# Performance work log

Hardware: AMD Instinct MI355X
Metric: run time of the kernel (lower is better)

## Reference

```python
import jax, jax.numpy as jnp
import numpy as np

EMBED_DIM = 1024
NUM_HEADS = 16
HEAD_DIM = EMBED_DIM // NUM_HEADS  # 64
SCALING = 0.125
T, B = 2048, 2


def setup_inputs() -> dict:
    key = jax.random.key(0)
    k_q, k_len, k_w1, k_b1, k_w2, k_b2 = jax.random.split(key, 6)
    query = jax.random.normal(k_q, (T, B, EMBED_DIM), dtype=jnp.float32)
    # realistic padding: each sequence has a valid length in [T//2, T)
    lengths = jax.random.randint(k_len, (B,), T // 2, T)
    key_padding_mask = jnp.arange(T)[None, :] >= lengths[:, None]  # [B, T] bool, True = pad
    s1 = 1.0 / np.sqrt(EMBED_DIM)
    W_in = jax.random.uniform(k_w1, (3 * EMBED_DIM, EMBED_DIM), jnp.float32, -s1, s1)
    b_in = jax.random.uniform(k_b1, (3 * EMBED_DIM,), jnp.float32, -s1, s1)
    W_out = jax.random.uniform(k_w2, (EMBED_DIM, EMBED_DIM), jnp.float32, -s1, s1)
    b_out = jax.random.uniform(k_b2, (EMBED_DIM,), jnp.float32, -s1, s1)
    return {"query": query, "key_padding_mask": key_padding_mask,
            "W_in": W_in, "b_in": b_in, "W_out": W_out, "b_out": b_out}


def reference(query, key_padding_mask, W_in, b_in, W_out, b_out):
    # query: [T, B, E]; key_padding_mask: [B, S] bool (True = padded key)
    t, b, e = query.shape
    h, hd = NUM_HEADS, HEAD_DIM
    proj = query @ W_in.T + b_in                      # [T, B, 3E]
    q, k, v = jnp.split(proj, 3, axis=-1)             # each [T, B, E]
    q = q * SCALING

    def to_bh(x):  # [T, B, E] -> [B*H, T, hd], matching torch view+transpose
        return x.reshape(t, b * h, hd).transpose(1, 0, 2)

    q, k, v = to_bh(q), to_bh(k), to_bh(v)
    attn_weights = jnp.einsum('bth,bsh->bts', q, k)   # [B*H, T, S]
    attn_weights = attn_weights.reshape(b, h, t, t)
    attn_weights = jnp.where(key_padding_mask[:, None, None, :], -jnp.inf, attn_weights)
    # softmax computed in float32 then cast back, as in the original
    attn_weights = jax.nn.softmax(attn_weights.astype(jnp.float32), axis=-1).astype(query.dtype)
    # dropout p=0 (eval/inference) -> identity
    attn = jnp.einsum('bhts,bhsd->bhtd', attn_weights, v.reshape(b, h, t, hd))  # [B,H,T,hd]
    attn = attn.reshape(b * h, t, hd).transpose(1, 0, 2).reshape(t, b, e)       # [T,B,E]
    return attn @ W_out.T + b_out
```

## Files before the change

kernel.cpp:

```cpp
#include <hip/hip_runtime.h>
#include <hip/hip_bf16.h>
#include <stdint.h>
#include <stddef.h>

typedef __hip_bfloat16 bf16;
typedef __attribute__((ext_vector_type(4))) float f32x4;
typedef __attribute__((ext_vector_type(8))) short s16x8;
typedef __attribute__((ext_vector_type(4))) short s16x4;

#define AS1 __attribute__((address_space(1)))
#define AS3 __attribute__((address_space(3)))

__device__ __forceinline__ void async_ld16(const void* g, void* l) {
  __builtin_amdgcn_global_load_lds((AS1 void*)g, (AS3 void*)l, 16, 0, 0);
}

__device__ __forceinline__ unsigned pk_bf16(float a, float b) {
  unsigned ua = __builtin_bit_cast(unsigned, a);
  unsigned ub = __builtin_bit_cast(unsigned, b);
  ua += 0x7FFFu + ((ua >> 16) & 1u);
  ub += 0x7FFFu + ((ub >> 16) & 1u);
  return (ua >> 16) | (ub & 0xFFFF0000u);
}

__global__ __launch_bounds__(256) void convert_all_kernel(const float* __restrict__ q_src,
                                                          const float* __restrict__ wi_src,
                                                          const float* __restrict__ wo_src,
                                                          bf16* __restrict__ q_dst,
                                                          bf16* __restrict__ wi_dst,
                                                          bf16* __restrict__ wo_dst,
                                                          const void* __restrict__ mask,
                                                          int* __restrict__ lengths) {
  int blk = blockIdx.x;
  if (blk >= 4096) {
    __shared__ int s_any;
    __shared__ int s_cnt[256];
    const int tid = threadIdx.x;
    const int b = blk - 4096;
    const unsigned char* m8 = (const unsigned char*)mask;
    if (tid == 0) s_any = 0;
    __syncthreads();
    int local = 0;
    for (int i = tid; i < 4096; i += 256) local |= m8[i];
    if (local) atomicOr(&s_any, 1);
    __syncthreads();
    int cnt = 0;
    if (s_any) {
      for (int t = tid; t < 2048; t += 256) cnt += (m8[b * 2048 + t] == 0) ? 1 : 0;
    } else {
      const int* m32 = (const int*)mask;
      for (int t = tid; t < 2048; t += 256) cnt += (m32[b * 2048 + t] == 0) ? 1 : 0;
    }
    s_cnt[tid] = cnt;
    __syncthreads();
    for (int s = 128; s > 0; s >>= 1) {
      if (tid < s) s_cnt[tid] += s_cnt[tid + s];
      __syncthreads();
    }
    if (tid == 0) lengths[b] = s_cnt[0];
    return;
  }
  const float* src;
  bf16* dst;
  int base;
  if (blk < 2048)      { src = q_src;  dst = q_dst;  base = blk * 2048; }
  else if (blk < 3584) { src = wi_src; dst = wi_dst; base = (blk - 2048) * 2048; }
  else                 { src = wo_src; dst = wo_dst; base = (blk - 3584) * 2048; }
  int i = base + threadIdx.x * 8;
  float4 a = *(const float4*)(src + i);
  float4 b = *(const float4*)(src + i + 4);
  bf16 t[8];
  t[0] = __float2bfloat16(a.x); t[1] = __float2bfloat16(a.y);
  t[2] = __float2bfloat16(a.z); t[3] = __float2bfloat16(a.w);
  t[4] = __float2bfloat16(b.x); t[5] = __float2bfloat16(b.y);
  t[6] = __float2bfloat16(b.z); t[7] = __float2bfloat16(b.w);
  *(s16x8*)(dst + i) = *(const s16x8*)t;
}

__device__ __forceinline__ void gemm_mainloop(const bf16* __restrict__ A,
                                              const bf16* __restrict__ Bm,
                                              bf16* As, bf16* Bs,
                                              int m0, int n0, f32x4 (&acc)[4][4]) {
  const int K = 1024;
  const int tid = threadIdx.x;
  const int wave = tid >> 6, lane = tid & 63;
  const int col = lane & 15, quad = lane >> 4;
  const int wm = wave & 1, wn = wave >> 1;
#pragma unroll
  for (int mi = 0; mi < 4; mi++)
#pragma unroll
    for (int ni = 0; ni < 4; ni++) acc[mi][ni] = (f32x4){0.f, 0.f, 0.f, 0.f};

  const int c0 = wave * 128 + lane;
  const int rowA0 = c0 >> 2, kc0 = (c0 & 3) * 8;
  const int c1 = c0 + 64;
  const int rowA1 = c1 >> 2, kc1 = (c1 & 3) * 8;
  char* ldsA0 = (char*)As + (size_t)(wave * 128) * 16;
  char* ldsA1 = ldsA0 + 64 * 16;
  char* ldsB0 = (char*)Bs + (size_t)(wave * 128) * 16;
  char* ldsB1 = ldsB0 + 64 * 16;
  const bf16* gA0 = A + (size_t)(m0 + rowA0) * K + kc0;
  const bf16* gA1 = A + (size_t)(m0 + rowA1) * K + kc1;
  const bf16* gB0 = Bm + (size_t)(n0 + rowA0) * K + kc0;
  const bf16* gB1 = Bm + (size_t)(n0 + rowA1) * K + kc1;

  for (int k0 = 0; k0 < K; k0 += 32) {
    async_ld16(gA0 + k0, ldsA0);
    async_ld16(gA1 + k0, ldsA1);
    async_ld16(gB0 + k0, ldsB0);
    async_ld16(gB1 + k0, ldsB1);
    __syncthreads();
    s16x8 af[4], bfr[4];
#pragma unroll
    for (int mi = 0; mi < 4; mi++)
      af[mi] = *(const s16x8*)(As + (wm * 64 + mi * 16 + col) * 32 + quad * 8);
#pragma unroll
    for (int ni = 0; ni < 4; ni++)
      bfr[ni] = *(const s16x8*)(Bs + (wn * 64 + ni * 16 + col) * 32 + quad * 8);
#pragma unroll
    for (int mi = 0; mi < 4; mi++)
#pragma unroll
      for (int ni = 0; ni < 4; ni++)
        acc[mi][ni] = __builtin_amdgcn_mfma_f32_16x16x32_bf16(af[mi], bfr[ni], acc[mi][ni], 0, 0, 0);
    __syncthreads();
  }
}

__global__ __launch_bounds__(256) void gemm_qkv(const bf16* __restrict__ X,
                                                const bf16* __restrict__ W,
                                                const float* __restrict__ bias,
                                                bf16* __restrict__ Qd,
                                                bf16* __restrict__ Kd,
                                                bf16* __restrict__ Vt) {
  __shared__ bf16 As[128 * 32];
  __shared__ bf16 Bs[128 * 32];
  const int m0 = blockIdx.y * 128, n0 = blockIdx.x * 128;
  f32x4 acc[4][4];
  gemm_mainloop(X, W, As, Bs, m0, n0, acc);
  const int tid = threadIdx.x;
  const int wave = tid >> 6, lane = tid & 63;
  const int col = lane & 15, quad = lane >> 4;
  const int wm = wave & 1, wn = wave >> 1;
  const float QSCALE = 0.125f * 1.4426950408889634f;
#pragma unroll
  for (int mi = 0; mi < 4; mi++)
#pragma unroll
    for (int ni = 0; ni < 4; ni++)
#pragma unroll
      for (int r = 0; r < 4; r++) {
        int m = m0 + wm * 64 + mi * 16 + quad * 4 + r;
        int n = n0 + wn * 64 + ni * 16 + col;
        float v = acc[mi][ni][r] + bias[n];
        int e = n & 1023, hh = e >> 6, d = e & 63;
        int t = m >> 1, b = m & 1;
        int bh = b * 16 + hh;
        if (n < 1024) {
          Qd[((size_t)bh * 2048 + t) * 64 + d] = __float2bfloat16(v * QSCALE);
        } else if (n < 2048) {
          Kd[((size_t)bh * 2048 + t) * 64 + d] = __float2bfloat16(v);
        } else {
          int sl = t & 63;
          int perm = ((sl >> 2) & 3) * 16 + (sl >> 4) * 4 + (sl & 3);
          Vt[(size_t)bh * 131072 + (t >> 6) * 4096 + d * 64 + perm] = __float2bfloat16(v);
        }
      }
}

__global__ __launch_bounds__(256, 4) void attn_kernel(const bf16* __restrict__ Qd,
                                                      const bf16* __restrict__ Kd,
                                                      const bf16* __restrict__ Vt,
                                                      const int* __restrict__ lengths,
                                                      bf16* __restrict__ attn_out) {
  __shared__ bf16 Ks[2][64 * 64];
  __shared__ bf16 Vs[2][64 * 64];

  const int bh = blockIdx.y;
  const int b = bh >> 4, h = bh & 15;
  const int qt0 = blockIdx.x * 64;
  const int tid = threadIdx.x;
  const int wave = tid >> 6, lane = tid & 63;
  const int col = lane & 15, quad = lane >> 4;
  const int len = lengths[b];
  const int nfull = len >> 6;
  const int rem = len & 63;
  const int nkt = nfull + (rem ? 1 : 0);

  const bf16* qptr = Qd + ((size_t)bh * 2048 + qt0 + wave * 16 + col) * 64 + quad * 8;
  const s16x8 bq0 = *(const s16x8*)(qptr);
  const s16x8 bq1 = *(const s16x8*)(qptr + 32);

  const int kbase0 = col * 128 + ((quad ^ (col & 7)) << 4);
  const int kbase1 = kbase0 ^ 64;
  const int vbase0 = col * 128 + (((quad << 1) ^ (col & 7)) << 4);
  const int vbase1 = vbase0 ^ 16;

  const bf16* Kg = Kd + (size_t)bh * 2048 * 64;
  const bf16* Vg = Vt + (size_t)bh * 131072;
  const int c0 = wave * 128 + lane, c1 = c0 + 64;
  const int r0 = c0 >> 3, j0 = (c0 & 7) ^ (r0 & 7);
  const int r1 = c1 >> 3, j1 = (c1 & 7) ^ (r1 & 7);
  const bf16* gK0 = Kg + r0 * 64 + j0 * 8;
  const bf16* gK1 = Kg + r1 * 64 + j1 * 8;
  const bf16* gV0 = Vg + r0 * 64 + j0 * 8;
  const bf16* gV1 = Vg + r1 * 64 + j1 * 8;
  const int dst0 = (wave * 128) * 16, dst1 = (wave * 128 + 64) * 16;

  auto stage = [&](int kt, int BUF) {
    const int off = kt * 4096;
    async_ld16(gK0 + off, (char*)Ks + BUF + dst0);
    async_ld16(gK1 + off, (char*)Ks + BUF + dst1);
    async_ld16(gV0 + off, (char*)Vs + BUF + dst0);
    async_ld16(gV1 + off, (char*)Vs + BUF + dst1);
  };

  const s16x4 aOnes = {0x3F80, 0x3F80, 0x3F80, 0x3F80};
  f32x4 lacc = (f32x4){0.f, 0.f, 0.f, 0.f};
  f32x4 oaccT[4];
#pragma unroll
  for (int dt = 0; dt < 4; dt++) oaccT[dt] = (f32x4){0.f, 0.f, 0.f, 0.f};

  auto tile = [&](int BUF, bool domask) {
    f32x4 sacc[4];
#pragma unroll
    for (int ti = 0; ti < 4; ti++) sacc[ti] = (f32x4){0.f, 0.f, 0.f, 0.f};
#pragma unroll
    for (int ti = 0; ti < 4; ti++) {
      const s16x8 ak0 = *(const s16x8*)((char*)Ks + BUF + ti * 2048 + kbase0);
      sacc[ti] = __builtin_amdgcn_mfma_f32_16x16x32_bf16(ak0, bq0, sacc[ti], 0, 0, 0);
      const s16x8 ak1 = *(const s16x8*)((char*)Ks + BUF + ti * 2048 + kbase1);
      sacc[ti] = __builtin_amdgcn_mfma_f32_16x16x32_bf16(ak1, bq1, sacc[ti], 0, 0, 0);
    }
    s16x4 bP[4];
#pragma unroll
    for (int ti = 0; ti < 4; ti++) {
      float p0 = exp2f(sacc[ti][0]);
      float p1 = exp2f(sacc[ti][1]);
      float p2 = exp2f(sacc[ti][2]);
      float p3 = exp2f(sacc[ti][3]);
      if (domask) {
        const int sb = ti * 16 + quad * 4;
        p0 = (sb + 0 < rem) ? p0 : 0.f;
        p1 = (sb + 1 < rem) ? p1 : 0.f;
        p2 = (sb + 2 < rem) ? p2 : 0.f;
        p3 = (sb + 3 < rem) ? p3 : 0.f;
      }
      uint2 u = {pk_bf16(p0, p1), pk_bf16(p2, p3)};
      bP[ti] = __builtin_bit_cast(s16x4, u);
    }
#pragma unroll
    for (int ti = 0; ti < 4; ti++)
      lacc = __builtin_amdgcn_mfma_f32_16x16x16bf16_1k(aOnes, bP[ti], lacc, 0, 0, 0);
#pragma unroll
    for (int dt = 0; dt < 4; dt++) {
#pragma unroll
      for (int sh = 0; sh < 2; sh++) {
        const s16x8 av = *(const s16x8*)((char*)Vs + BUF + dt * 2048 + (sh ? vbase1 : vbase0));
        const s16x4 alo = __builtin_shufflevector(av, av, 0, 1, 2, 3);
        const s16x4 ahi = __builtin_shufflevector(av, av, 4, 5, 6, 7);
        oaccT[dt] = __builtin_amdgcn_mfma_f32_16x16x16bf16_1k(alo, bP[sh * 2], oaccT[dt], 0, 0, 0);
        oaccT[dt] = __builtin_amdgcn_mfma_f32_16x16x16bf16_1k(ahi, bP[sh * 2 + 1], oaccT[dt], 0, 0, 0);
      }
    }
  };

  stage(0, 0);
  __syncthreads();
  int kt = 0;
  for (;;) {
    if (kt + 1 < nkt) stage(kt + 1, 8192);
    tile(0, kt >= nfull);
    __syncthreads();
    if (++kt >= nkt) break;
    if (kt + 1 < nkt) stage(kt + 1, 0);
    tile(8192, kt >= nfull);
    __syncthreads();
    if (++kt >= nkt) break;
  }

  const float linv = 1.0f / lacc[0];
  const int t = qt0 + wave * 16 + col;
  bf16* outp = attn_out + ((size_t)t * 2 + b) * 1024 + h * 64 + quad * 4;
#pragma unroll
  for (int dt = 0; dt < 4; dt++) {
    uint2 u = {pk_bf16(oaccT[dt][0] * linv, oaccT[dt][1] * linv),
               pk_bf16(oaccT[dt][2] * linv, oaccT[dt][3] * linv)};
    *(uint2*)(outp + dt * 16) = u;
  }
}

__global__ __launch_bounds__(256) void gemm_out(const bf16* __restrict__ Aa,
                                                const bf16* __restrict__ W,
                                                const float* __restrict__ bias,
                                                float* __restrict__ out) {
  __shared__ bf16 As[128 * 32];
  __shared__ bf16 Bs[128 * 32];
  const int m0 = blockIdx.y * 128, n0 = blockIdx.x * 128;
  f32x4 acc[4][4];
  gemm_mainloop(Aa, W, As, Bs, m0, n0, acc);
  const int tid = threadIdx.x;
  const int wave = tid >> 6, lane = tid & 63;
  const int col = lane & 15, quad = lane >> 4;
  const int wm = wave & 1, wn = wave >> 1;
#pragma unroll
  for (int mi = 0; mi < 4; mi++)
#pragma unroll
    for (int ni = 0; ni < 4; ni++)
#pragma unroll
      for (int r = 0; r < 4; r++) {
        int m = m0 + wm * 64 + mi * 16 + quad * 4 + r;
        int n = n0 + wn * 64 + ni * 16 + col;
        out[(size_t)m * 1024 + n] = acc[mi][ni][r] + bias[n];
      }
}

extern "C" void kernel_launch(void* const* d_in, const int* in_sizes, int n_in,
                              void* d_out, int out_size, void* d_ws, size_t ws_size,
                              hipStream_t stream) {
  (void)in_sizes; (void)n_in; (void)out_size; (void)ws_size;
  const float* query = (const float*)d_in[0];
  const void*  mask  = d_in[1];
  const float* W_in  = (const float*)d_in[2];
  const float* b_in  = (const float*)d_in[3];
  const float* W_out = (const float*)d_in[4];
  const float* b_out = (const float*)d_in[5];
  float* out = (float*)d_out;

  char* ws = (char*)d_ws;
  bf16* Xbf    = (bf16*)(ws);
  bf16* attnb  = (bf16*)(ws);
  bf16* Winbf  = (bf16*)(ws + 8388608);
  bf16* Woutbf = (bf16*)(ws + 8388608 + 6291456);
  bf16* Qd     = (bf16*)(ws + 16777216);
  bf16* Kd     = (bf16*)(ws + 25165824);
  bf16* Vt     = (bf16*)(ws + 33554432);
  int*  lens   = (int*)(ws + 41943040);

  convert_all_kernel<<<4098, 256, 0, stream>>>(query, W_in, W_out, Xbf, Winbf, Woutbf,
                                               mask, lens);
  gemm_qkv<<<dim3(24, 32), 256, 0, stream>>>(Xbf, Winbf, b_in, Qd, Kd, Vt);
  attn_kernel<<<dim3(32, 32), 256, 0, stream>>>(Qd, Kd, Vt, lens, attnb);
  gemm_out<<<dim3(8, 32), 256, 0, stream>>>(attnb, Woutbf, b_out, out);
}
```

Before: 215.3 us.

## Split attention tile paths, use fast exp2 and truncation, retile output GEMM

Attention tiles are split into a masked and an unmasked path, so full tiles skip the per-element mask selects. The exponent uses the hardware exp2 builtin, and packing to bf16 becomes a truncating byte permute instead of round-to-nearest, which slightly changes numerics. The output projection GEMM is rewritten with 64x128 tiles and single-buffered async loads over a doubled grid, to give more blocks and better occupancy. The fp32-to-bf16 conversion kernel now uses the manual packed rounding helper.

```diff
diff --git a/kernel.cpp b/kernel.cpp
--- a/kernel.cpp
+++ b/kernel.cpp
@@ -14,6 +14,12 @@
 __device__ __forceinline__ void async_ld16(const void* g, void* l) {
   __builtin_amdgcn_global_load_lds((AS1 void*)g, (AS3 void*)l, 16, 0, 0);
 }
+
+#if __has_builtin(__builtin_amdgcn_exp2f)
+#define EXP2F(x) __builtin_amdgcn_exp2f(x)
+#else
+#define EXP2F(x) exp2f(x)
+#endif
 
 __device__ __forceinline__ unsigned pk_bf16(float a, float b) {
   unsigned ua = __builtin_bit_cast(unsigned, a);
@@ -21,6 +27,11 @@
   ua += 0x7FFFu + ((ua >> 16) & 1u);
   ub += 0x7FFFu + ((ub >> 16) & 1u);
   return (ua >> 16) | (ub & 0xFFFF0000u);
+}
+
+__device__ __forceinline__ unsigned pk_trunc(float a, float b) {
+  return __builtin_amdgcn_perm(__builtin_bit_cast(unsigned, b),
+                               __builtin_bit_cast(unsigned, a), 0x07060302u);
 }
 
 __global__ __launch_bounds__(256) void convert_all_kernel(const float* __restrict__ q_src,
@@ -69,12 +80,10 @@
   int i = base + threadIdx.x * 8;
   float4 a = *(const float4*)(src + i);
   float4 b = *(const float4*)(src + i + 4);
-  bf16 t[8];
-  t[0] = __float2bfloat16(a.x); t[1] = __float2bfloat16(a.y);
-  t[2] = __float2bfloat16(a.z); t[3] = __float2bfloat16(a.w);
-  t[4] = __float2bfloat16(b.x); t[5] = __float2bfloat16(b.y);
-  t[6] = __float2bfloat16(b.z); t[7] = __float2bfloat16(b.w);
-  *(s16x8*)(dst + i) = *(const s16x8*)t;
+  unsigned u[4];
+  u[0] = pk_bf16(a.x, a.y); u[1] = pk_bf16(a.z, a.w);
+  u[2] = pk_bf16(b.x, b.y); u[3] = pk_bf16(b.z, b.w);
+  *(uint4*)(dst + i) = *(const uint4*)u;
 }
 
 __device__ __forceinline__ void gemm_mainloop(const bf16* __restrict__ A,
@@ -214,39 +223,22 @@
   };
 
   const s16x4 aOnes = {0x3F80, 0x3F80, 0x3F80, 0x3F80};
-  f32x4 lacc = (f32x4){0.f, 0.f, 0.f, 0.f};
+  const f32x4 Zf = (f32x4){0.f, 0.f, 0.f, 0.f};
+  f32x4 lacc = Zf;
   f32x4 oaccT[4];
 #pragma unroll
-  for (int dt = 0; dt < 4; dt++) oaccT[dt] = (f32x4){0.f, 0.f, 0.f, 0.f};
-
-  auto tile = [&](int BUF, bool domask) {
-    f32x4 sacc[4];
-#pragma unroll
-    for (int ti = 0; ti < 4; ti++) sacc[ti] = (f32x4){0.f, 0.f, 0.f, 0.f};
+  for (int dt = 0; dt < 4; dt++) oaccT[dt] = Zf;
+
+  auto score = [&](int BUF, f32x4 (&sacc)[4]) {
 #pragma unroll
     for (int ti = 0; ti < 4; ti++) {
       const s16x8 ak0 = *(const s16x8*)((char*)Ks + BUF + ti * 2048 + kbase0);
-      sacc[ti] = __builtin_amdgcn_mfma_f32_16x16x32_bf16(ak0, bq0, sacc[ti], 0, 0, 0);
+      sacc[ti] = __builtin_amdgcn_mfma_f32_16x16x32_bf16(ak0, bq0, Zf, 0, 0, 0);
       const s16x8 ak1 = *(const s16x8*)((char*)Ks + BUF + ti * 2048 + kbase1);
       sacc[ti] = __builtin_amdgcn_mfma_f32_16x16x32_bf16(ak1, bq1, sacc[ti], 0, 0, 0);
     }
-    s16x4 bP[4];
-#pragma unroll
-    for (int ti = 0; ti < 4; ti++) {
-      float p0 = exp2f(sacc[ti][0]);
-      float p1 = exp2f(sacc[ti][1]);
-      float p2 = exp2f(sacc[ti][2]);
-      float p3 = exp2f(sacc[ti][3]);
-      if (domask) {
-        const int sb = ti * 16 + quad * 4;
-        p0 = (sb + 0 < rem) ? p0 : 0.f;
-        p1 = (sb + 1 < rem) ? p1 : 0.f;
-        p2 = (sb + 2 < rem) ? p2 : 0.f;
-        p3 = (sb + 3 < rem) ? p3 : 0.f;
-      }
-      uint2 u = {pk_bf16(p0, p1), pk_bf16(p2, p3)};
-      bP[ti] = __builtin_bit_cast(s16x4, u);
-    }
+  };
+  auto accum = [&](int BUF, s16x4 (&bP)[4]) {
 #pragma unroll
     for (int ti = 0; ti < 4; ti++)
       lacc = __builtin_amdgcn_mfma_f32_16x16x16bf16_1k(aOnes, bP[ti], lacc, 0, 0, 0);
@@ -263,16 +255,46 @@
     }
   };
 
+  auto tile_full = [&](int BUF) {
+    f32x4 sacc[4];
+    score(BUF, sacc);
+    s16x4 bP[4];
+#pragma unroll
+    for (int ti = 0; ti < 4; ti++) {
+      uint2 u = {pk_trunc(EXP2F(sacc[ti][0]), EXP2F(sacc[ti][1])),
+                 pk_trunc(EXP2F(sacc[ti][2]), EXP2F(sacc[ti][3]))};
+      bP[ti] = __builtin_bit_cast(s16x4, u);
+    }
+    accum(BUF, bP);
+  };
+
+  auto tile_mask = [&](int BUF) {
+    f32x4 sacc[4];
+    score(BUF, sacc);
+    s16x4 bP[4];
+#pragma unroll
+    for (int ti = 0; ti < 4; ti++) {
+      const int sb = ti * 16 + quad * 4;
+      float p0 = (sb + 0 < rem) ? EXP2F(sacc[ti][0]) : 0.f;
+      float p1 = (sb + 1 < rem) ? EXP2F(sacc[ti][1]) : 0.f;
+      float p2 = (sb + 2 < rem) ? EXP2F(sacc[ti][2]) : 0.f;
+      float p3 = (sb + 3 < rem) ? EXP2F(sacc[ti][3]) : 0.f;
+      uint2 u = {pk_trunc(p0, p1), pk_trunc(p2, p3)};
+      bP[ti] = __builtin_bit_cast(s16x4, u);
+    }
+    accum(BUF, bP);
+  };
+
   stage(0, 0);
   __syncthreads();
   int kt = 0;
   for (;;) {
     if (kt + 1 < nkt) stage(kt + 1, 8192);
-    tile(0, kt >= nfull);
+    if (kt < nfull) tile_full(0); else tile_mask(0);
     __syncthreads();
     if (++kt >= nkt) break;
     if (kt + 1 < nkt) stage(kt + 1, 0);
-    tile(8192, kt >= nfull);
+    if (kt < nfull) tile_full(8192); else tile_mask(8192);
     __syncthreads();
     if (++kt >= nkt) break;
   }
@@ -292,25 +314,51 @@
                                                 const bf16* __restrict__ W,
                                                 const float* __restrict__ bias,
                                                 float* __restrict__ out) {
-  __shared__ bf16 As[128 * 32];
   __shared__ bf16 Bs[128 * 32];
-  const int m0 = blockIdx.y * 128, n0 = blockIdx.x * 128;
-  f32x4 acc[4][4];
-  gemm_mainloop(Aa, W, As, Bs, m0, n0, acc);
+  __shared__ bf16 As[64 * 32];
+  const int K = 1024;
+  const int m0 = blockIdx.y * 64, n0 = blockIdx.x * 128;
   const int tid = threadIdx.x;
   const int wave = tid >> 6, lane = tid & 63;
   const int col = lane & 15, quad = lane >> 4;
-  const int wm = wave & 1, wn = wave >> 1;
-#pragma unroll
-  for (int mi = 0; mi < 4; mi++)
-#pragma unroll
-    for (int ni = 0; ni < 4; ni++)
-#pragma unroll
-      for (int r = 0; r < 4; r++) {
-        int m = m0 + wm * 64 + mi * 16 + quad * 4 + r;
-        int n = n0 + wn * 64 + ni * 16 + col;
-        out[(size_t)m * 1024 + n] = acc[mi][ni][r] + bias[n];
-      }
+
+  f32x4 acc[8];
+#pragma unroll
+  for (int ni = 0; ni < 8; ni++) acc[ni] = (f32x4){0.f, 0.f, 0.f, 0.f};
+
+  const int cB0 = wave * 64 + lane, cB1 = cB0 + 256;
+  const int rB0 = cB0 >> 2, kB0 = (cB0 & 3) * 8;
+  const int rB1 = cB1 >> 2, kB1 = (cB1 & 3) * 8;
+  const bf16* gB0 = W + (size_t)(n0 + rB0) * K + kB0;
+  const bf16* gB1 = W + (size_t)(n0 + rB1) * K + kB1;
+  char* ldsB0 = (char*)Bs + (size_t)(wave * 64) * 16;
+  char* ldsB1 = (char*)Bs + (size_t)(256 + wave * 64) * 16;
+  const int rA = cB0 >> 2, kA = (cB0 & 3) * 8;
+  const bf16* gA = Aa + (size_t)(m0 + rA) * K + kA;
+  char* ldsA = (char*)As + (size_t)(wave * 64) * 16;
+
+  for (int k0 = 0; k0 < K; k0 += 32) {
+    async_ld16(gB0 + k0, ldsB0);
+    async_ld16(gB1 + k0, ldsB1);
+    async_ld16(gA + k0, ldsA);
+    __syncthreads();
+    const s16x8 af = *(const s16x8*)(As + (wave * 16 + col) * 32 + quad * 8);
+#pragma unroll
+    for (int ni = 0; ni < 8; ni++) {
+      const s16x8 bfr = *(const s16x8*)(Bs + (ni * 16 + col) * 32 + quad * 8);
+      acc[ni] = __builtin_amdgcn_mfma_f32_16x16x32_bf16(af, bfr, acc[ni], 0, 0, 0);
+    }
+    __syncthreads();
+  }
+
+#pragma unroll
+  for (int ni = 0; ni < 8; ni++)
+#pragma unroll
+    for (int r = 0; r < 4; r++) {
+      int m = m0 + wave * 16 + quad * 4 + r;
+      int n = n0 + ni * 16 + col;
+      out[(size_t)m * 1024 + n] = acc[ni][r] + bias[n];
+    }
 }
 
 extern "C" void kernel_launch(void* const* d_in, const int* in_sizes, int n_in,
@@ -339,5 +387,5 @@
                                                mask, lens);
   gemm_qkv<<<dim3(24, 32), 256, 0, stream>>>(Xbf, Winbf, b_in, Qd, Kd, Vt);
   attn_kernel<<<dim3(32, 32), 256, 0, stream>>>(Qd, Kd, Vt, lens, attnb);
-  gemm_out<<<dim3(8, 32), 256, 0, stream>>>(attnb, Woutbf, b_out, out);
-}
+  gemm_out<<<dim3(8, 64), 256, 0, stream>>>(attnb, Woutbf, b_out, out);
+}
```

Measured after the change: 198.2 us. 1.09x faster.
